# Performance work log

Hardware: AMD Instinct MI355X
Metric: run time of the kernel (lower is better)

## Reference

```python
import jax, jax.numpy as jnp
import numpy as np

CHNN = 1024
K = 2048


def _conv1x1(W, b, x):
    # x: (B, C_in, L), W: (C_out, C_in), b: (C_out,)
    return jnp.einsum('oc,bcl->bol', W, x) + b[None, :, None]


def setup_inputs() -> dict:
    key = jax.random.key(0)
    ks = jax.random.split(key, 10)
    s = 0.02
    return {
        'vc': jax.random.normal(ks[0], (1, CHNN, K), dtype=jnp.float32),
        'vm': jax.random.normal(ks[1], (1, CHNN, K), dtype=jnp.float32),
        'W_ak': jax.random.normal(ks[2], (K, CHNN), dtype=jnp.float32) * s,
        'b_ak': jax.random.normal(ks[3], (K,), dtype=jnp.float32) * s,
        'W_c': jax.random.normal(ks[4], (CHNN, CHNN), dtype=jnp.float32) * s,
        'b_c': jax.random.normal(ks[5], (CHNN,), dtype=jnp.float32) * s,
        'W_mad': jax.random.normal(ks[6], (CHNN, CHNN), dtype=jnp.float32) * s,
        'b_mad': jax.random.normal(ks[7], (CHNN,), dtype=jnp.float32) * s,
        'W_gcn': jax.random.normal(ks[8], (CHNN, CHNN), dtype=jnp.float32) * s,
        'b_gcn': jax.random.normal(ks[9], (CHNN,), dtype=jnp.float32) * s,
    }


def reference(vc, vm, W_ak, b_ak, W_c, b_c, W_mad, b_mad, W_gcn, b_gcn):
    # vcw: (1, K, L) assignment logits; softmax over the K (channel) dim
    vcw = _conv1x1(W_ak, b_ak, vc)
    vcw = jax.nn.softmax(vcw, axis=1)
    w = vcw[0].T                      # (L, K)  (batch forced to 1 by squeeze(0))
    # vm features: (1, CHNN, K)
    vmr = jax.nn.relu(_conv1x1(W_c, b_c, vm))
    # F.linear(vm, w): contract last dim (K) with w's second dim -> (1, CHNN, L)
    vma = jnp.einsum('bck,lk->bcl', vmr, w)
    vma = _conv1x1(W_mad, b_mad, vma)  # (1, CHNN, L)
    # dense adjacency over positions: (1, L, L)
    A = jnp.einsum('bck,bcl->bkl', vma, vma)
    # GCN: x (1, K, CHNN) @ W + b, then softmax(A) @ x  (requires L == K)
    x = jnp.swapaxes(vmr, 1, 2) @ W_gcn + b_gcn
    A = jax.nn.softmax(A, axis=-1)
    out = A @ x                        # (1, L, CHNN)
    return jnp.swapaxes(out, 1, 2)     # (1, CHNN, L)
```

## Files before the change

kernel.cpp:

```cpp
#include <hip/hip_runtime.h>
#include <hip/hip_bf16.h>


typedef __bf16 bf16x4 __attribute__((ext_vector_type(4)));
typedef __bf16 bf16x8 __attribute__((ext_vector_type(8)));
typedef float  f32x4  __attribute__((ext_vector_type(4)));

typedef const void __attribute__((address_space(1)))* gptr_t;
typedef void       __attribute__((address_space(3)))* lptr_t;

__device__ __forceinline__ void load16_lds(const __bf16* g, __bf16* l)
{
    __builtin_amdgcn_global_load_lds((gptr_t)g, (lptr_t)l, 16, 0, 0);
}

template<typename OT, int TM_, int TN_, int BIAS_, bool RELU_, int STORE_>
struct GC {
    using OUT_T = OT;
    static constexpr int TM = TM_, TN = TN_, BIAS = BIAS_, STORE = STORE_;
    static constexpr bool RELU = RELU_;
    static constexpr int SMEM = 2 * (TM_ + TN_) * 32 * 2;
};

template<class CF>
__device__ __forceinline__ void gemm_body(
    int bid, char* smem,
    const __bf16* __restrict__ A, const __bf16* __restrict__ B,
    const float* __restrict__ bias,
    typename CF::OUT_T* __restrict__ C, typename CF::OUT_T* __restrict__ CT,
    int M, int N, int K, int ntx)
{
    constexpr int TM = CF::TM, TN = CF::TN;
    constexpr int FM = TM / 32, FN = TN / 32;
    constexpr int NA = TM / 64, NB = TN / 64;
    __bf16* sA = (__bf16*)smem;
    __bf16* sB = (__bf16*)smem + 2 * TM * 32;
    const int tid = threadIdx.x, lane = tid & 63, wv = tid >> 6;
    const int m0 = (bid / ntx) * TM, n0 = (bid % ntx) * TN;
    const int mw = (wv >> 1) * (FM * 16), nw = (wv & 1) * (FN * 16);

    f32x4 acc[FM][FN];
    #pragma unroll
    for (int i = 0; i < FM; ++i)
        #pragma unroll
        for (int j = 0; j < FN; ++j)
            acc[i][j] = (f32x4){0.f, 0.f, 0.f, 0.f};

    const __bf16* gA = A + (size_t)m0 * K;
    const __bf16* gB = B + (size_t)n0 * K;

    auto stage = [&](int k0, int buf) {
        #pragma unroll
        for (int i = 0; i < NA; ++i) {
            const int c = (wv * NA + i) * 64 + lane;
            load16_lds(gA + (size_t)(c >> 2) * K + k0 + (c & 3) * 8,
                       &sA[buf * TM * 32 + (wv * NA + i) * 512]);
        }
        #pragma unroll
        for (int i = 0; i < NB; ++i) {
            const int c = (wv * NB + i) * 64 + lane;
            load16_lds(gB + (size_t)(c >> 2) * K + k0 + (c & 3) * 8,
                       &sB[buf * TN * 32 + (wv * NB + i) * 512]);
        }
    };

    stage(0, 0);
    int cur = 0;
    for (int k0 = 0; k0 < K; k0 += 32) {
        __syncthreads();
        if (k0 + 32 < K) stage(k0 + 32, cur ^ 1);
        bf16x8 af[FM], bfr[FN];
        #pragma unroll
        for (int i = 0; i < FM; ++i)
            af[i] = *(const bf16x8*)&sA[cur * TM * 32 + (mw + i * 16 + (lane & 15)) * 32 + (lane >> 4) * 8];
        #pragma unroll
        for (int j = 0; j < FN; ++j)
            bfr[j] = *(const bf16x8*)&sB[cur * TN * 32 + (nw + j * 16 + (lane & 15)) * 32 + (lane >> 4) * 8];
        #pragma unroll
        for (int i = 0; i < FM; ++i)
            #pragma unroll
            for (int j = 0; j < FN; ++j)
                acc[i][j] = __builtin_amdgcn_mfma_f32_16x16x32_bf16(af[i], bfr[j], acc[i][j], 0, 0, 0);
        cur ^= 1;
    }

    #pragma unroll
    for (int i = 0; i < FM; ++i) {
        const int rowb = m0 + mw + i * 16 + (lane >> 4) * 4;
        #pragma unroll
        for (int j = 0; j < FN; ++j) {
            const int col = n0 + nw + j * 16 + (lane & 15);
            f32x4 v = acc[i][j];
            #pragma unroll
            for (int r = 0; r < 4; ++r) {
                float f = v[r];
                if (CF::BIAS == 1) f += bias[rowb + r];
                if (CF::BIAS == 2) f += bias[col];
                if (CF::RELU) f = fmaxf(f, 0.f);
                v[r] = f;
            }
            if (CF::STORE == 0 || CF::STORE == 2) {
                #pragma unroll
                for (int r = 0; r < 4; ++r)
                    C[(size_t)(rowb + r) * N + col] = (typename CF::OUT_T)v[r];
            }
            if (CF::STORE == 1 || CF::STORE == 2) {
                if constexpr (sizeof(typename CF::OUT_T) == 4) {
                    *(f32x4*)&CT[(size_t)col * M + rowb] = v;
                } else {
                    bf16x4 w = { (__bf16)v[0], (__bf16)v[1], (__bf16)v[2], (__bf16)v[3] };
                    *(bf16x4*)&CT[(size_t)col * M + rowb] = w;
                }
            }
        }
    }
}

template<class CF>
__global__ __launch_bounds__(256, 2)
void gemm1(const __bf16* __restrict__ A, const __bf16* __restrict__ B,
           const float* __restrict__ bias,
           typename CF::OUT_T* __restrict__ C, typename CF::OUT_T* __restrict__ CT,
           int M, int N, int K, int ntx)
{
    __shared__ char smem[CF::SMEM];
    gemm_body<CF>(blockIdx.x, smem, A, B, bias, C, CT, M, N, K, ntx);
}

template<class C1, class C2>
__global__ __launch_bounds__(256, 2)
void gemm2(int nblk1,
           const __bf16* __restrict__ A1, const __bf16* __restrict__ B1,
           const float* __restrict__ b1,
           typename C1::OUT_T* __restrict__ C1p, typename C1::OUT_T* __restrict__ CT1,
           int M1, int N1, int K1, int ntx1,
           const __bf16* __restrict__ A2, const __bf16* __restrict__ B2,
           const float* __restrict__ b2,
           typename C2::OUT_T* __restrict__ C2p, typename C2::OUT_T* __restrict__ CT2,
           int M2, int N2, int K2, int ntx2)
{
    constexpr int S = C1::SMEM > C2::SMEM ? C1::SMEM : C2::SMEM;
    __shared__ char smem[S];
    if ((int)blockIdx.x < nblk1)
        gemm_body<C1>(blockIdx.x, smem, A1, B1, b1, C1p, CT1, M1, N1, K1, ntx1);
    else
        gemm_body<C2>(blockIdx.x - nblk1, smem, A2, B2, b2, C2p, CT2, M2, N2, K2, ntx2);
}

__device__ __forceinline__ void tp_tile(const float* __restrict__ in,
                                        __bf16* __restrict__ outp,
                                        int R, int C, int bx, int by)
{
    __shared__ float t[32][33];
    const int tx = threadIdx.x & 31, ty = threadIdx.x >> 5;
    #pragma unroll
    for (int i = ty; i < 32; i += 8)
        t[i][tx] = in[(size_t)(by + i) * C + (bx + tx)];
    __syncthreads();
    #pragma unroll
    for (int i = ty; i < 32; i += 8)
        outp[(size_t)(bx + i) * R + (by + tx)] = (__bf16)t[tx][i];
}

__device__ __forceinline__ void cast_blk(const float* __restrict__ s,
                                         __bf16* __restrict__ d, int blk)
{
    const int i = blk * 1024 + threadIdx.x * 4;
    float4 v = *(const float4*)&s[i];
    bf16x4 w = { (__bf16)v.x, (__bf16)v.y, (__bf16)v.z, (__bf16)v.w };
    *(bf16x4*)&d[i] = w;
}

__device__ __forceinline__ void softmax_row(__bf16* __restrict__ p)
{
    __shared__ float red[256];
    const int t = threadIdx.x;
    bf16x8 v = *(bf16x8*)&p[t * 8];
    float f[8];
    float m = -1e30f;
    #pragma unroll
    for (int r = 0; r < 8; ++r) { f[r] = (float)v[r]; m = fmaxf(m, f[r]); }
    red[t] = m;
    __syncthreads();
    for (int s = 128; s > 0; s >>= 1) {
        if (t < s) red[t] = fmaxf(red[t], red[t + s]);
        __syncthreads();
    }
    m = red[0];
    __syncthreads();
    float sum = 0.f;
    #pragma unroll
    for (int r = 0; r < 8; ++r) { f[r] = expf(f[r] - m); sum += f[r]; }
    red[t] = sum;
    __syncthreads();
    for (int s = 128; s > 0; s >>= 1) {
        if (t < s) red[t] += red[t + s];
        __syncthreads();
    }
    const float inv = 1.f / red[0];
    bf16x8 w;
    #pragma unroll
    for (int r = 0; r < 8; ++r) w[r] = (__bf16)(f[r] * inv);
    *(bf16x8*)&p[t * 8] = w;
}

__global__ __launch_bounds__(256)
void prep(const float* __restrict__ vc, __bf16* __restrict__ vcT,
          const float* __restrict__ vm, __bf16* __restrict__ vmT,
          const float* __restrict__ W_ak, __bf16* __restrict__ W_akb,
          const float* __restrict__ W_c, __bf16* __restrict__ W_cb,
          const float* __restrict__ W_mad, __bf16* __restrict__ W_madb,
          const float* __restrict__ W_gcn, __bf16* __restrict__ W_gcnT)
{
    const int x = blockIdx.x;
    if (blockIdx.z == 0) {
        const float* in = (x < 2048) ? vc : vm;
        __bf16* o       = (x < 2048) ? vcT : vmT;
        const int e = x & 2047;
        tp_tile(in, o, 1024, 2048, (e & 63) * 32, (e >> 6) * 32);
    } else if (blockIdx.z == 1) {
        if (x < 2048)      cast_blk(W_ak, W_akb, x);
        else if (x < 3072) cast_blk(W_c, W_cb, x - 2048);
        else               cast_blk(W_mad, W_madb, x - 3072);
    } else {
        if (x >= 1024) return;
        tp_tile(W_gcn, W_gcnT, 1024, 1024, (x & 31) * 32, (x >> 5) * 32);
    }
}

__global__ __launch_bounds__(256)
void row_softmax_k(__bf16* __restrict__ A)
{
    softmax_row(A + (size_t)blockIdx.x * 2048);
}

extern "C" void kernel_launch(void* const* d_in, const int* in_sizes, int n_in,
                              void* d_out, int out_size, void* d_ws, size_t ws_size,
                              hipStream_t stream)
{
    const float* vc    = (const float*)d_in[0];
    const float* vm    = (const float*)d_in[1];
    const float* W_ak  = (const float*)d_in[2];
    const float* b_ak  = (const float*)d_in[3];
    const float* W_c   = (const float*)d_in[4];
    const float* b_c   = (const float*)d_in[5];
    const float* W_mad = (const float*)d_in[6];
    const float* b_mad = (const float*)d_in[7];
    const float* W_gcn = (const float*)d_in[8];
    const float* b_gcn = (const float*)d_in[9];
    float* out = (float*)d_out;

    char* ws = (char*)d_ws;
    const size_t MB = 1u << 20;
    __bf16* ST     = (__bf16*)(ws);
    __bf16* P      = (__bf16*)(ws);
    __bf16* vcT    = (__bf16*)(ws + 8 * MB);
    __bf16* vma1T  = (__bf16*)(ws + 8 * MB);
    __bf16* W_akb  = (__bf16*)(ws + 12 * MB);
    __bf16* vmaT   = (__bf16*)(ws + 12 * MB);
    __bf16* vmT    = (__bf16*)(ws + 16 * MB);
    __bf16* xT     = (__bf16*)(ws + 16 * MB);
    __bf16* W_cb   = (__bf16*)(ws + 20 * MB);
    __bf16* W_madb = (__bf16*)(ws + 22 * MB);
    __bf16* vmr    = (__bf16*)(ws + 24 * MB);
    __bf16* vmrT   = (__bf16*)(ws + 28 * MB);
    __bf16* W_gcnT = (__bf16*)(ws + 20 * MB);
    W_gcnT = (__bf16*)((char*)d_out + 0);

    using G3  = GC<__bf16, 128, 64, 2, false, 0>;
    using G5  = GC<__bf16, 128, 64, 1, true,  2>;
    using G7  = GC<__bf16, 128, 64, 0, false, 0>;
    using G11 = GC<__bf16, 128, 64, 1, false, 0>;
    using G8  = GC<__bf16, 64,  64, 2, false, 0>;
    using G9  = GC<__bf16, 128, 64, 0, false, 0>;
    using G12 = GC<float,  64,  64, 0, false, 1>;

    prep<<<dim3(4096, 1, 3), 256, 0, stream>>>(vc, vcT, vm, vmT, W_ak, W_akb,
                                               W_c, W_cb, W_mad, W_madb,
                                               W_gcn, W_gcnT);
    gemm2<G3, G5><<<768, 256, 0, stream>>>(512,
        vcT, W_akb, b_ak, ST, (__bf16*)nullptr, 2048, 2048, 1024, 32,
        W_cb, vmT, b_c, vmr, vmrT, 1024, 2048, 1024, 32);
    row_softmax_k<<<2048, 256, 0, stream>>>(ST);
    gemm2<G7, G11><<<512, 256, 0, stream>>>(256,
        ST, vmr, nullptr, vma1T, (__bf16*)nullptr, 2048, 1024, 2048, 16,
        W_gcnT, vmrT, b_gcn, xT, (__bf16*)nullptr, 1024, 2048, 1024, 32);
    gemm1<G8><<<512, 256, 0, stream>>>(vma1T, W_madb, b_mad, vmaT, (__bf16*)nullptr,
                                       2048, 1024, 1024, 16);
    gemm1<G9><<<512, 256, 0, stream>>>(vmaT, vmaT, nullptr, P, (__bf16*)nullptr,
                                       2048, 2048, 1024, 32);
    row_softmax_k<<<2048, 256, 0, stream>>>(P);
    gemm1<G12><<<512, 256, 0, stream>>>(P, xT, nullptr, (float*)nullptr, out,
                                        2048, 1024, 2048, 16);
}
```

Before: 214.6 us.

## Reassociate W_mad before assignment matmul and fuse softmax into GEMM launch

Reorders W_mad·(vmr·S^T) as (W_mad·vmr)·S^T, so the W_mad product no longer depends on the softmax output. That product and the GCN x projection now run in one launch together with the assignment-logit softmax rows as extra blocks, which removes one kernel launch and one dependency barrier. The W_mad bias is folded into the later GEMM epilogue. W_gcnT moves from the output buffer into workspace, and the first GEMM no longer writes the non-transposed vmr.

```diff
diff --git a/kernel.cpp b/kernel.cpp
--- a/kernel.cpp
+++ b/kernel.cpp
@@ -147,30 +147,6 @@
         gemm_body<C2>(blockIdx.x - nblk1, smem, A2, B2, b2, C2p, CT2, M2, N2, K2, ntx2);
 }
 
-__device__ __forceinline__ void tp_tile(const float* __restrict__ in,
-                                        __bf16* __restrict__ outp,
-                                        int R, int C, int bx, int by)
-{
-    __shared__ float t[32][33];
-    const int tx = threadIdx.x & 31, ty = threadIdx.x >> 5;
-    #pragma unroll
-    for (int i = ty; i < 32; i += 8)
-        t[i][tx] = in[(size_t)(by + i) * C + (bx + tx)];
-    __syncthreads();
-    #pragma unroll
-    for (int i = ty; i < 32; i += 8)
-        outp[(size_t)(bx + i) * R + (by + tx)] = (__bf16)t[tx][i];
-}
-
-__device__ __forceinline__ void cast_blk(const float* __restrict__ s,
-                                         __bf16* __restrict__ d, int blk)
-{
-    const int i = blk * 1024 + threadIdx.x * 4;
-    float4 v = *(const float4*)&s[i];
-    bf16x4 w = { (__bf16)v.x, (__bf16)v.y, (__bf16)v.z, (__bf16)v.w };
-    *(bf16x4*)&d[i] = w;
-}
-
 __device__ __forceinline__ void softmax_row(__bf16* __restrict__ p)
 {
     __shared__ float red[256];
@@ -202,6 +178,56 @@
     #pragma unroll
     for (int r = 0; r < 8; ++r) w[r] = (__bf16)(f[r] * inv);
     *(bf16x8*)&p[t * 8] = w;
+}
+
+template<class C1, class C2>
+__global__ __launch_bounds__(256, 2)
+void gemm2sm(int nblk1, int nblk2,
+             const __bf16* __restrict__ A1, const __bf16* __restrict__ B1,
+             const float* __restrict__ b1,
+             typename C1::OUT_T* __restrict__ C1p,
+             int M1, int N1, int K1, int ntx1,
+             const __bf16* __restrict__ A2, const __bf16* __restrict__ B2,
+             const float* __restrict__ b2,
+             typename C2::OUT_T* __restrict__ C2p,
+             int M2, int N2, int K2, int ntx2,
+             __bf16* __restrict__ SM)
+{
+    constexpr int S = C1::SMEM > C2::SMEM ? C1::SMEM : C2::SMEM;
+    __shared__ char smem[S];
+    const int b = blockIdx.x;
+    if (b < nblk1)
+        gemm_body<C1>(b, smem, A1, B1, b1, C1p, (typename C1::OUT_T*)nullptr,
+                      M1, N1, K1, ntx1);
+    else if (b < nblk1 + nblk2)
+        gemm_body<C2>(b - nblk1, smem, A2, B2, b2, C2p, (typename C2::OUT_T*)nullptr,
+                      M2, N2, K2, ntx2);
+    else
+        softmax_row(SM + (size_t)(b - nblk1 - nblk2) * 2048);
+}
+
+__device__ __forceinline__ void tp_tile(const float* __restrict__ in,
+                                        __bf16* __restrict__ outp,
+                                        int R, int C, int bx, int by)
+{
+    __shared__ float t[32][33];
+    const int tx = threadIdx.x & 31, ty = threadIdx.x >> 5;
+    #pragma unroll
+    for (int i = ty; i < 32; i += 8)
+        t[i][tx] = in[(size_t)(by + i) * C + (bx + tx)];
+    __syncthreads();
+    #pragma unroll
+    for (int i = ty; i < 32; i += 8)
+        outp[(size_t)(bx + i) * R + (by + tx)] = (__bf16)t[tx][i];
+}
+
+__device__ __forceinline__ void cast_blk(const float* __restrict__ s,
+                                         __bf16* __restrict__ d, int blk)
+{
+    const int i = blk * 1024 + threadIdx.x * 4;
+    float4 v = *(const float4*)&s[i];
+    bf16x4 w = { (__bf16)v.x, (__bf16)v.y, (__bf16)v.z, (__bf16)v.w };
+    *(bf16x4*)&d[i] = w;
 }
 
 __global__ __launch_bounds__(256)
@@ -255,23 +281,21 @@
     __bf16* ST     = (__bf16*)(ws);
     __bf16* P      = (__bf16*)(ws);
     __bf16* vcT    = (__bf16*)(ws + 8 * MB);
-    __bf16* vma1T  = (__bf16*)(ws + 8 * MB);
+    __bf16* vmaT   = (__bf16*)(ws + 8 * MB);
     __bf16* W_akb  = (__bf16*)(ws + 12 * MB);
-    __bf16* vmaT   = (__bf16*)(ws + 12 * MB);
+    __bf16* vmm    = (__bf16*)(ws + 12 * MB);
     __bf16* vmT    = (__bf16*)(ws + 16 * MB);
     __bf16* xT     = (__bf16*)(ws + 16 * MB);
     __bf16* W_cb   = (__bf16*)(ws + 20 * MB);
     __bf16* W_madb = (__bf16*)(ws + 22 * MB);
-    __bf16* vmr    = (__bf16*)(ws + 24 * MB);
-    __bf16* vmrT   = (__bf16*)(ws + 28 * MB);
-    __bf16* W_gcnT = (__bf16*)(ws + 20 * MB);
-    W_gcnT = (__bf16*)((char*)d_out + 0);
+    __bf16* vmrT   = (__bf16*)(ws + 24 * MB);
+    __bf16* W_gcnT = (__bf16*)(ws + 28 * MB);
 
     using G3  = GC<__bf16, 128, 64, 2, false, 0>;
-    using G5  = GC<__bf16, 128, 64, 1, true,  2>;
-    using G7  = GC<__bf16, 128, 64, 0, false, 0>;
+    using G5  = GC<__bf16, 128, 64, 1, true,  1>;
+    using G6  = GC<__bf16, 128, 64, 0, false, 0>;
     using G11 = GC<__bf16, 128, 64, 1, false, 0>;
-    using G8  = GC<__bf16, 64,  64, 2, false, 0>;
+    using G7  = GC<__bf16, 64,  64, 2, false, 0>;
     using G9  = GC<__bf16, 128, 64, 0, false, 0>;
     using G12 = GC<float,  64,  64, 0, false, 1>;
 
@@ -280,13 +304,13 @@
                                                W_gcn, W_gcnT);
     gemm2<G3, G5><<<768, 256, 0, stream>>>(512,
         vcT, W_akb, b_ak, ST, (__bf16*)nullptr, 2048, 2048, 1024, 32,
-        W_cb, vmT, b_c, vmr, vmrT, 1024, 2048, 1024, 32);
-    row_softmax_k<<<2048, 256, 0, stream>>>(ST);
-    gemm2<G7, G11><<<512, 256, 0, stream>>>(256,
-        ST, vmr, nullptr, vma1T, (__bf16*)nullptr, 2048, 1024, 2048, 16,
-        W_gcnT, vmrT, b_gcn, xT, (__bf16*)nullptr, 1024, 2048, 1024, 32);
-    gemm1<G8><<<512, 256, 0, stream>>>(vma1T, W_madb, b_mad, vmaT, (__bf16*)nullptr,
-                                       2048, 1024, 1024, 16);
+        W_cb, vmT, b_c, (__bf16*)nullptr, vmrT, 1024, 2048, 1024, 32);
+    gemm2sm<G6, G11><<<2560, 256, 0, stream>>>(256, 256,
+        W_madb, vmrT, nullptr, vmm, 1024, 2048, 1024, 32,
+        W_gcnT, vmrT, b_gcn, xT, 1024, 2048, 1024, 32,
+        ST);
+    gemm1<G7><<<512, 256, 0, stream>>>(ST, vmm, b_mad, vmaT, (__bf16*)nullptr,
+                                       2048, 1024, 2048, 16);
     gemm1<G9><<<512, 256, 0, stream>>>(vmaT, vmaT, nullptr, P, (__bf16*)nullptr,
                                        2048, 2048, 1024, 32);
     row_softmax_k<<<2048, 256, 0, stream>>>(P);
```

Result: no change. 211.3 us (-1.6%).
